# Optimization experiments

Measured on AMD Instinct MI355X. Metric: run time of the kernel, lower is better.

Reference implementation:

```python
import jax, jax.numpy as jnp
import numpy as np
from jax import lax

H = 512          # hidden_dim
U = H // 2       # GRU units per direction
L = 3            # num_layers
B = 64           # num sequences
T = 512          # timesteps per sequence
EXTRA = 1000     # pass-through tail rows in `states`
RATE = 0.1       # dropout_rate
WSCALE = 0.05


def setup_inputs() -> dict:
    key = jax.random.key(0)
    ks = jax.random.split(key, 9)
    N = B * T + EXTRA
    states = jax.random.normal(ks[0], (N, H), jnp.float32)
    # prefix-valid mask: each sequence has a random valid length in [1, T]
    lengths = jax.random.randint(ks[1], (B,), 1, T + 1)
    mask2d = jnp.arange(T)[None, :] < lengths[:, None]          # [B, T]
    mask = jnp.concatenate([mask2d.reshape(-1), jnp.zeros((EXTRA,), bool)])
    # per-layer, per-direction GRU params (Keras reset_after=True layout):
    # kernel [H, 3U] (z|r|h), recurrent [U, 3U], bias [2, 3U] (input bias, recurrent bias)
    Wf = jax.random.normal(ks[2], (L, H, 3 * U), jnp.float32) * WSCALE
    Uf = jax.random.normal(ks[3], (L, U, 3 * U), jnp.float32) * WSCALE
    bf = jnp.zeros((L, 2, 3 * U), jnp.float32)
    Wb = jax.random.normal(ks[4], (L, H, 3 * U), jnp.float32) * WSCALE
    Ub = jax.random.normal(ks[5], (L, U, 3 * U), jnp.float32) * WSCALE
    bb = jnp.zeros((L, 2, 3 * U), jnp.float32)
    return {
        "states": states, "mask": mask, "seq_shape": (B, T), "training": 1,
        "Wf": Wf, "Uf": Uf, "bf": bf, "Wb": Wb, "Ub": Ub, "bb": bb,
    }


def _gru_scan(x, m, W, Uw, b):
    """Keras GRU (reset_after=True) over time with Keras mask semantics.
    x: [T, B, H], m: [T, B] bool. Returns outputs [T, B, U].
    Masked steps carry state (output = previous output)."""
    bi, br = b[0], b[1]
    xp = jnp.einsum('tbh,hk->tbk', x, W) + bi   # [T, B, 3U], hoisted input proj
    h0 = jnp.zeros((x.shape[1], U), x.dtype)

    def step(h, inp):
        xp_t, m_t = inp
        hp = h @ Uw + br                         # [B, 3U]
        xz, xr, xh = jnp.split(xp_t, 3, axis=-1)
        hz, hr, hh = jnp.split(hp, 3, axis=-1)
        z = jax.nn.sigmoid(xz + hz)
        r = jax.nn.sigmoid(xr + hr)
        hcand = jnp.tanh(xh + r * hh)
        hn = z * h + (1.0 - z) * hcand
        hn = jnp.where(m_t[:, None], hn, h)      # carry state through masked steps
        return hn, hn

    _, ys = lax.scan(step, h0, (xp, m))
    return ys


def _forward(states, mask, seq_shape, training, Wf, Uf, bf, Wb, Ub, bb):
    Bn, Tn = int(seq_shape[0]), int(seq_shape[1])
    total = Bn * Tn
    x = states[:total].reshape(Bn, Tn, H).transpose(1, 0, 2)  # [T, B, H]
    m = mask[:total].reshape(Bn, Tn).T                        # [T, B]
    rate = RATE * float(bool(training))
    dkey = jax.random.key(1234)
    for l in range(L):
        yf = _gru_scan(x, m, Wf[l], Uf[l], bf[l])
        yb = jnp.flip(_gru_scan(jnp.flip(x, 0), jnp.flip(m, 0), Wb[l], Ub[l], bb[l]), 0)
        x = jnp.concatenate([yf, yb], axis=-1)                # [T, B, H]
        if rate > 0.0:
            dkey, sk = jax.random.split(dkey)
            keep = jax.random.bernoulli(sk, 1.0 - rate, x.shape)
            x = jnp.where(keep, x / (1.0 - rate), 0.0)
    out = x.transpose(1, 0, 2).reshape(-1, H)                 # [B*T, H]
    return jnp.concatenate([out, states[total:]], axis=0)


def reference(states, mask, seq_shape, training, Wf, Uf, bf, Wb, Ub, bb):
    return _forward(states, mask, seq_shape, training, Wf, Uf, bf, Wb, Ub, bb)
```

## Files before the change

kernel.cpp:

```cpp
#include <hip/hip_runtime.h>
#include <stdint.h>

typedef __attribute__((ext_vector_type(8))) short short8;
typedef __attribute__((ext_vector_type(4))) float f32x4;

#define XB16_OFF  0UL
#define XP_OFF    33554432UL
#define WT_OFF    134217728UL
#define UT_OFF    138936320UL
#define BIASC_OFF 141295616UL
#define BRC_OFF   141314048UL
#define MASKT_OFF 141332480UL
#define FLAG_OFF  141725760UL

#define HB_STRIDE 264
#define HBLK (16 * HB_STRIDE)
#define LDS_BYTES (((size_t)256 * HB_STRIDE + 2 * HBLK) * 2)

#define LDS_BARRIER() asm volatile("s_waitcnt lgkmcnt(0)\n\ts_barrier" ::: "memory")

__host__ __device__ static inline void tf2x32(unsigned k0, unsigned k1,
                                              unsigned x0, unsigned x1,
                                              unsigned* o0, unsigned* o1) {
  unsigned ks2 = k0 ^ k1 ^ 0x1BD11BDAu;
#define TFR(r) { x0 += x1; x1 = (x1 << (r)) | (x1 >> (32 - (r))); x1 ^= x0; }
  x0 += k0; x1 += k1;
  TFR(13) TFR(15) TFR(26) TFR(6)   x0 += k1;  x1 += ks2 + 1u;
  TFR(17) TFR(29) TFR(16) TFR(24)  x0 += ks2; x1 += k0 + 2u;
  TFR(13) TFR(15) TFR(26) TFR(6)   x0 += k0;  x1 += k1 + 3u;
  TFR(17) TFR(29) TFR(16) TFR(24)  x0 += k1;  x1 += ks2 + 4u;
  TFR(13) TFR(15) TFR(26) TFR(6)   x0 += ks2; x1 += k0 + 5u;
#undef TFR
  *o0 = x0; *o1 = x1;
}

__device__ static inline short f2bf(float f) {
  unsigned u = __float_as_uint(f);
  u = (u + 0x7fffu + ((u >> 16) & 1u)) >> 16;
  return (short)u;
}
__device__ static inline float bf2f(short s) {
  unsigned u = ((unsigned)(unsigned short)s) << 16;
  return __uint_as_float(u);
}
__device__ static inline float cvt_lo(unsigned d) {
  union { unsigned short u; _Float16 h; } c; c.u = (unsigned short)(d & 0xffffu);
  return (float)c.h;
}
__device__ static inline float cvt_hi(unsigned d) {
  union { unsigned short u; _Float16 h; } c; c.u = (unsigned short)(d >> 16);
  return (float)c.h;
}

__global__ void init_k(unsigned* flag) {
  if (threadIdx.x == 0) *flag = 0u;
}

__global__ __launch_bounds__(256) void prep_k(
    const float* __restrict__ states, const unsigned* __restrict__ maskw,
    const float* __restrict__ Wf, const float* __restrict__ Uf,
    const float* __restrict__ bf_, const float* __restrict__ Wb,
    const float* __restrict__ Ub, const float* __restrict__ bb_,
    short* __restrict__ xb16, float* __restrict__ dout,
    short* __restrict__ Wt, short* __restrict__ Ut,
    float* __restrict__ biasc, float* __restrict__ brc,
    unsigned* __restrict__ flag) {
  const unsigned gid = blockIdx.x * 256 + threadIdx.x;
  {
    unsigned c = gid & 511u, rw = gid >> 9;
    unsigned t = rw >> 6, b = rw & 63u;
    xb16[gid] = f2bf(states[(size_t)(b * 512 + t) * 512 + c]);
  }
  if (gid < 512000u) dout[16777216u + gid] = states[16777216u + gid];
  if (gid < 2359296u) {
    unsigned l = gid / 786432u, rem = gid % 786432u;
    unsigned n = rem >> 9, k = rem & 511u;
    float s = (n < 768u) ? Wf[(size_t)(l * 512 + k) * 768 + n]
                         : Wb[(size_t)(l * 512 + k) * 768 + (n - 768u)];
    Wt[gid] = f2bf(s);
  }
  if (gid < 1179648u) {
    unsigned g = gid / 196608u, rem = gid % 196608u;
    unsigned dirv = g / 3u, l = g % 3u;
    unsigned n = rem >> 8, k = rem & 255u;
    const float* Usrc = dirv ? Ub : Uf;
    Ut[gid] = f2bf(Usrc[(size_t)(l * 256 + k) * 768 + n]);
  }
  if (gid < 4608u) {
    unsigned l = gid / 1536u, n = gid % 1536u;
    unsigned dirv = n / 768u, rem = n % 768u;
    const float* bsrc = dirv ? bb_ : bf_;
    float v = bsrc[(l * 2 + 0) * 768 + rem];
    if (rem < 512u) v += bsrc[(l * 2 + 1) * 768 + rem];
    biasc[gid] = v;
  }
  if (gid < 4608u) {
    unsigned g = gid / 768u, n = gid % 768u;
    unsigned dirv = g / 3u, l = g % 3u;
    brc[gid] = (dirv ? bb_ : bf_)[(l * 2 + 1) * 768 + n];
  }
  if (gid < 8192u) {
    if (maskw[gid] > 1u) atomicOr(flag, 1u);
  }
}

__global__ __launch_bounds__(256) void maskt_k(
    const unsigned char* __restrict__ mask8, const unsigned* __restrict__ flagp,
    unsigned char* __restrict__ maskt) {
  const unsigned gid = blockIdx.x * 256 + threadIdx.x;
  const unsigned b = gid >> 9, t = gid & 511u;
  const bool mbyte = (*flagp) != 0u;
  unsigned v = mbyte ? (unsigned)mask8[gid] : ((const unsigned*)mask8)[gid];
  maskt[t * 64 + b] = v ? 1u : 0u;
}

__global__ __launch_bounds__(256) void proj_gemm(
    const short* __restrict__ A, const short* __restrict__ Bt,
    const float* __restrict__ bias, _Float16* __restrict__ C) {
  __shared__ __align__(16) short As[4096];
  __shared__ __align__(16) short Bs[4096];
  const int tid = threadIdx.x;
  const int wave = tid >> 6, lane = tid & 63;
  const int col = lane & 15, kq = lane >> 4;
  const int wr = wave >> 1, wc = wave & 1;
  const int m0 = blockIdx.x * 128, n0 = blockIdx.y * 128;
  const uint4* Aq = (const uint4*)A;
  const uint4* Bq = (const uint4*)Bt;
  uint4* AsQ = (uint4*)As;
  uint4* BsQ = (uint4*)Bs;
  f32x4 acc[4][4];
#pragma unroll
  for (int i = 0; i < 4; ++i)
#pragma unroll
    for (int j = 0; j < 4; ++j) acc[i][j] = (f32x4){0.f, 0.f, 0.f, 0.f};

  for (int kt = 0; kt < 16; ++kt) {
    const int k8 = kt * 4;
#pragma unroll
    for (int rnd = 0; rnd < 2; ++rnd) {
      int chunk = rnd * 256 + tid;
      int row = chunk >> 2, kc = chunk & 3;
      AsQ[chunk] = Aq[(size_t)(m0 + row) * 64 + k8 + kc];
      BsQ[chunk] = Bq[(size_t)(n0 + row) * 64 + k8 + kc];
    }
    __syncthreads();
    short8 af[4], bfv[4];
#pragma unroll
    for (int i = 0; i < 4; ++i)
      af[i] = *(const short8*)(As + (wr * 64 + i * 16 + col) * 32 + kq * 8);
#pragma unroll
    for (int j = 0; j < 4; ++j)
      bfv[j] = *(const short8*)(Bs + (wc * 64 + j * 16 + col) * 32 + kq * 8);
#pragma unroll
    for (int i = 0; i < 4; ++i)
#pragma unroll
      for (int j = 0; j < 4; ++j)
        acc[i][j] = __builtin_amdgcn_mfma_f32_16x16x32_bf16(af[i], bfv[j], acc[i][j], 0, 0, 0);
    __syncthreads();
  }
#pragma unroll
  for (int j = 0; j < 4; ++j) {
    const int cg = n0 + wc * 64 + j * 16 + col;
    const float bv = bias[cg];
    const int dirv = cg / 768, rem = cg % 768;
    const int gate = rem >> 8, u = rem & 255;
    const int w = u >> 4, c = u & 15;
    const int colofs = dirv * 768 +
        ((gate < 2) ? (w * 32 + c * 2 + gate) : (512 + w * 16 + c));
#pragma unroll
    for (int i = 0; i < 4; ++i) {
      const int rb = m0 + wr * 64 + i * 16 + kq * 4;
#pragma unroll
      for (int r = 0; r < 4; ++r)
        C[(size_t)(rb + r) * 1536 + colofs] = (_Float16)(acc[i][j][r] + bv);
    }
  }
}

__global__ __launch_bounds__(1024, 4) void gru16(
    const _Float16* __restrict__ xp, const short* __restrict__ UtAll,
    const float* __restrict__ brcAll, const unsigned char* __restrict__ maskt,
    short* __restrict__ yout, int layer) {
  extern __shared__ short lds[];
  short* hgate = lds;
  short* hbuf  = lds + 256 * HB_STRIDE;

  const int bid = blockIdx.x;
  const int dir = bid >> 2;
  const int b0 = (bid & 3) * 16;
  const int tid = threadIdx.x;
  const int wave = tid >> 6, lane = tid & 63;
  const int col = lane & 15, quad = lane >> 4;
  const int u = wave * 16 + col;
  const short* Ut = UtAll + (size_t)(dir * 3 + layer) * 768 * 256;
  const float* brc = brcAll + (dir * 3 + layer) * 768;

  const short* Uth = Ut + 512 * 256;
  for (int c = tid; c < 8192; c += 1024) {
    int row = c >> 5, q = c & 31;
    *(uint4*)(hgate + row * HB_STRIDE + q * 8) = *(const uint4*)(Uth + row * 256 + q * 8);
  }
  for (int i = tid; i < 2 * HBLK; i += 1024) hbuf[i] = 0;

  short8 zB[8], rB[8];
#pragma unroll
  for (int ks = 0; ks < 8; ++ks) {
    zB[ks] = *(const short8*)(Ut + (size_t)u * 256 + ks * 32 + quad * 8);
    rB[ks] = *(const short8*)(Ut + (size_t)(256 + u) * 256 + ks * 32 + quad * 8);
  }
  const float brh = brc[512 + u];

  const int t0 = dir ? 511 : 0;
  const int tstep = dir ? -1 : 1;
  const int xstep = tstep * 64 * 3072;
  const char* xpb = (const char*)xp;
  const int row0 = (t0 * 64 + b0 + quad * 4);
  unsigned xzrA = (unsigned)(row0 * 3072 + dir * 1536 + wave * 64 + col * 4);
  unsigned xzrB = xzrA + 6144u;
  unsigned xhA  = (unsigned)(row0 * 3072 + dir * 1536 + 1024 + wave * 32 + col * 2);
  unsigned xhB  = xhA + 6144u;

  const short* hgB = hgate + u * HB_STRIDE + quad * 8;
  const int rd_lane = col * HB_STRIDE + quad * 8;
  const int wr_lane = (quad * 4) * HB_STRIDE + u;

  unsigned yoff = (unsigned)(row0 * 1024 + dir * 512 + u * 2);
  const int ystep = tstep * 65536;
  int moff = t0 * 64 + b0 + quad * 4;

  unsigned pzr[4], ph[4], pmc;
  pzr[0] = *(const unsigned*)(xpb + xzrA);
  pzr[1] = *(const unsigned*)(xpb + xzrA + 3072);
  pzr[2] = *(const unsigned*)(xpb + xzrB);
  pzr[3] = *(const unsigned*)(xpb + xzrB + 3072);
  ph[0] = *(const unsigned short*)(xpb + xhA);
  ph[1] = *(const unsigned short*)(xpb + xhA + 3072);
  ph[2] = *(const unsigned short*)(xpb + xhB);
  ph[3] = *(const unsigned short*)(xpb + xhB + 3072);
  pmc = *(const unsigned*)(maskt + moff);

  float hp[4] = {0.f, 0.f, 0.f, 0.f};
  __syncthreads();

  for (int s = 0; s < 512; ++s) {
    f32x4 az, ar, ah;
#pragma unroll
    for (int r = 0; r < 4; ++r) {
      az[r] = cvt_lo(pzr[r]);
      ar[r] = cvt_hi(pzr[r]);
      ah[r] = brh;
    }
    if (s < 511) {
      xzrA += xstep; xzrB += xstep; xhA += xstep; xhB += xstep;
      pzr[0] = *(const unsigned*)(xpb + xzrA);
      pzr[1] = *(const unsigned*)(xpb + xzrA + 3072);
      pzr[2] = *(const unsigned*)(xpb + xzrB);
      pzr[3] = *(const unsigned*)(xpb + xzrB + 3072);
    }

    const short* hrd = hbuf + (s & 1) * HBLK + rd_lane;
#pragma unroll
    for (int ks = 0; ks < 8; ++ks) {
      short8 a  = *(const short8*)(hrd + ks * 32);
      short8 hb = *(const short8*)(hgB + ks * 32);
      az = __builtin_amdgcn_mfma_f32_16x16x32_bf16(a, zB[ks], az, 0, 0, 0);
      ar = __builtin_amdgcn_mfma_f32_16x16x32_bf16(a, rB[ks], ar, 0, 0, 0);
      ah = __builtin_amdgcn_mfma_f32_16x16x32_bf16(a, hb,     ah, 0, 0, 0);
    }

    short* hwr = hbuf + ((s & 1) ^ 1) * HBLK + wr_lane;
    char* yb = (char*)yout + yoff;
#pragma unroll
    for (int r = 0; r < 4; ++r) {
      float z  = 1.f / (1.f + __expf(-az[r]));
      float rr = 1.f / (1.f + __expf(-ar[r]));
      float xh = cvt_lo(ph[r]);
      float pre = xh + rr * ah[r];
      float hc = 1.f - 2.f / (__expf(2.f * pre) + 1.f);
      float hpv = hp[r];
      float hn = hc + z * (hpv - hc);
      hn = ((pmc >> (8 * r)) & 0xffu) ? hn : hpv;
      hp[r] = hn;
      short hnb = f2bf(hn);
      hwr[r * HB_STRIDE] = hnb;
      *(short*)(yb + r * 1024) = hnb;
    }
    yoff += ystep;
    if (s < 511) {
      ph[0] = *(const unsigned short*)(xpb + xhA);
      ph[1] = *(const unsigned short*)(xpb + xhA + 3072);
      ph[2] = *(const unsigned short*)(xpb + xhB);
      ph[3] = *(const unsigned short*)(xpb + xhB + 3072);
      moff += tstep * 64;
      pmc = *(const unsigned*)(maskt + moff);
    }
    LDS_BARRIER();
  }
}

__global__ __launch_bounds__(256) void drop_k(
    short* __restrict__ xb16, float* __restrict__ dout,
    const int* __restrict__ training, unsigned k0, unsigned k1, int last) {
  const unsigned gid = blockIdx.x * 256 + threadIdx.x;
  float v = bf2f(xb16[gid]);
  unsigned y0, y1;
  tf2x32(k0, k1, 0u, gid, &y0, &y1);
  unsigned bits = y0 ^ y1;
  float u = __uint_as_float((bits >> 9) | 0x3f800000u) - 1.0f;
  bool keep = u < 0.9f;
  int tr = *training;
  float ov = tr ? (keep ? v * (1.0f / 0.9f) : 0.0f) : v;
  if (last) {
    unsigned r = gid >> 9, c = gid & 511u;
    unsigned t = r >> 6, b = r & 63u;
    dout[(size_t)(b * 512 + t) * 512 + c] = ov;
  } else {
    xb16[gid] = f2bf(ov);
  }
}

extern "C" void kernel_launch(void* const* d_in, const int* in_sizes, int n_in,
                              void* d_out, int out_size, void* d_ws, size_t ws_size,
                              hipStream_t stream) {
  (void)in_sizes; (void)n_in; (void)out_size; (void)ws_size;
  const float* states = (const float*)d_in[0];
  const void*  mask   = d_in[1];
  const int*   training = (const int*)d_in[3];
  const float* Wf = (const float*)d_in[4];
  const float* Uf = (const float*)d_in[5];
  const float* bf_ = (const float*)d_in[6];
  const float* Wb = (const float*)d_in[7];
  const float* Ub = (const float*)d_in[8];
  const float* bb_ = (const float*)d_in[9];
  char* ws = (char*)d_ws;

  short* xb16   = (short*)(ws + XB16_OFF);
  _Float16* xp  = (_Float16*)(ws + XP_OFF);
  short* Wt     = (short*)(ws + WT_OFF);
  short* Ut     = (short*)(ws + UT_OFF);
  float* biasc  = (float*)(ws + BIASC_OFF);
  float* brc    = (float*)(ws + BRC_OFF);
  unsigned char* maskt = (unsigned char*)(ws + MASKT_OFF);
  unsigned* flag = (unsigned*)(ws + FLAG_OFF);
  float* dout = (float*)d_out;

  hipFuncSetAttribute((const void*)gru16,
                      hipFuncAttributeMaxDynamicSharedMemorySize, (int)LDS_BYTES);

  unsigned d0 = 0u, d1 = 1234u, sk0[3], sk1[3];
  for (int l = 0; l < 3; ++l) {
    unsigned a, b, c, d;
    tf2x32(d0, d1, 0u, 0u, &a, &b);
    tf2x32(d0, d1, 0u, 1u, &c, &d);
    sk0[l] = c; sk1[l] = d;
    d0 = a; d1 = b;
  }

  init_k<<<1, 64, 0, stream>>>(flag);
  prep_k<<<65536, 256, 0, stream>>>(states, (const unsigned*)mask, Wf, Uf, bf_,
                                    Wb, Ub, bb_, xb16, dout, Wt, Ut, biasc, brc, flag);
  maskt_k<<<128, 256, 0, stream>>>((const unsigned char*)mask, flag, maskt);
  for (int l = 0; l < 3; ++l) {
    proj_gemm<<<dim3(256, 12), 256, 0, stream>>>(xb16, Wt + (size_t)l * 1536 * 512,
                                                 biasc + l * 1536, xp);
    gru16<<<8, 1024, LDS_BYTES, stream>>>(xp, Ut, brc, maskt, xb16, l);
    drop_k<<<65536, 256, 0, stream>>>(xb16, dout, training, sk0[l], sk1[l], l == 2);
  }
}
```

Before: 4.129 ms.

## Transpose GRU recurrent MFMA so each lane owns four consecutive units

The recurrent matmul operands are swapped so weights become the A operand and the hidden state the B operand. Each lane now holds four consecutive hidden units for one sequence. The input projection GEMM writes its output in a matching per-timestep, per-direction layout, so each lane loads gate inputs with three 8-byte loads. Hidden-state writes to LDS and to the output are packed into one 8-byte store per lane using v_cvt_pk_bf16_f32, and the sigmoid and tanh now call exp2 directly. This is meant to cut the number of narrow scattered global loads and stores on the serial critical path. It relies on the GEMM epilogue and the GRU kernel agreeing on the new xp layout.

```diff
diff --git a/kernel.cpp b/kernel.cpp
--- a/kernel.cpp
+++ b/kernel.cpp
@@ -164,15 +164,13 @@
     const float bv = bias[cg];
     const int dirv = cg / 768, rem = cg % 768;
     const int gate = rem >> 8, u = rem & 255;
-    const int w = u >> 4, c = u & 15;
-    const int colofs = dirv * 768 +
-        ((gate < 2) ? (w * 32 + c * 2 + gate) : (512 + w * 16 + c));
+    const size_t cbase =
+        ((size_t)(((m0 >> 6) + wr) * 2 + dirv)) * 49152 + gate * 256 + u;
 #pragma unroll
     for (int i = 0; i < 4; ++i) {
-      const int rb = m0 + wr * 64 + i * 16 + kq * 4;
 #pragma unroll
       for (int r = 0; r < 4; ++r)
-        C[(size_t)(rb + r) * 1536 + colofs] = (_Float16)(acc[i][j][r] + bv);
+        C[cbase + (size_t)(i * 16 + kq * 4 + r) * 768] = (_Float16)(acc[i][j][r] + bv);
     }
   }
 }
@@ -191,7 +189,7 @@
   const int tid = threadIdx.x;
   const int wave = tid >> 6, lane = tid & 63;
   const int col = lane & 15, quad = lane >> 4;
-  const int u = wave * 16 + col;
+  const int u0 = wave * 16 + quad * 4;
   const short* Ut = UtAll + (size_t)(dir * 3 + layer) * 768 * 256;
   const float* brc = brcAll + (dir * 3 + layer) * 768;
 
@@ -202,98 +200,89 @@
   }
   for (int i = tid; i < 2 * HBLK; i += 1024) hbuf[i] = 0;
 
-  short8 zB[8], rB[8];
+  short8 zA[8], rA[8];
 #pragma unroll
   for (int ks = 0; ks < 8; ++ks) {
-    zB[ks] = *(const short8*)(Ut + (size_t)u * 256 + ks * 32 + quad * 8);
-    rB[ks] = *(const short8*)(Ut + (size_t)(256 + u) * 256 + ks * 32 + quad * 8);
-  }
-  const float brh = brc[512 + u];
+    zA[ks] = *(const short8*)(Ut + (size_t)(wave * 16 + col) * 256 + ks * 32 + quad * 8);
+    rA[ks] = *(const short8*)(Ut + (size_t)(256 + wave * 16 + col) * 256 + ks * 32 + quad * 8);
+  }
+  f32x4 brh;
+#pragma unroll
+  for (int r = 0; r < 4; ++r) brh[r] = brc[512 + u0 + r];
 
   const int t0 = dir ? 511 : 0;
   const int tstep = dir ? -1 : 1;
-  const int xstep = tstep * 64 * 3072;
   const char* xpb = (const char*)xp;
-  const int row0 = (t0 * 64 + b0 + quad * 4);
-  unsigned xzrA = (unsigned)(row0 * 3072 + dir * 1536 + wave * 64 + col * 4);
-  unsigned xzrB = xzrA + 6144u;
-  unsigned xhA  = (unsigned)(row0 * 3072 + dir * 1536 + 1024 + wave * 32 + col * 2);
-  unsigned xhB  = xhA + 6144u;
-
-  const short* hgB = hgate + u * HB_STRIDE + quad * 8;
+  const int gb = b0 + col;
+  unsigned xaddr = (unsigned)(((t0 * 2 + dir) * 64 + gb) * 1536 + wave * 32 + quad * 8);
+  const int xstep = tstep * 196608;
+
+  const short* hgA = hgate + (wave * 16 + col) * HB_STRIDE + quad * 8;
   const int rd_lane = col * HB_STRIDE + quad * 8;
-  const int wr_lane = (quad * 4) * HB_STRIDE + u;
-
-  unsigned yoff = (unsigned)(row0 * 1024 + dir * 512 + u * 2);
+  const int wr_lane = col * HB_STRIDE + u0;
+
+  unsigned yoff = (unsigned)((t0 * 64 + gb) * 1024 + dir * 512 + u0 * 2);
   const int ystep = tstep * 65536;
-  int moff = t0 * 64 + b0 + quad * 4;
-
-  unsigned pzr[4], ph[4], pmc;
-  pzr[0] = *(const unsigned*)(xpb + xzrA);
-  pzr[1] = *(const unsigned*)(xpb + xzrA + 3072);
-  pzr[2] = *(const unsigned*)(xpb + xzrB);
-  pzr[3] = *(const unsigned*)(xpb + xzrB + 3072);
-  ph[0] = *(const unsigned short*)(xpb + xhA);
-  ph[1] = *(const unsigned short*)(xpb + xhA + 3072);
-  ph[2] = *(const unsigned short*)(xpb + xhB);
-  ph[3] = *(const unsigned short*)(xpb + xhB + 3072);
-  pmc = *(const unsigned*)(maskt + moff);
+  int moff = t0 * 64 + gb;
+
+  uint2 pz, pr, ph;
+  unsigned pm;
+  pz = *(const uint2*)(xpb + xaddr);
+  pr = *(const uint2*)(xpb + xaddr + 512);
+  ph = *(const uint2*)(xpb + xaddr + 1024);
+  pm = maskt[moff];
 
   float hp[4] = {0.f, 0.f, 0.f, 0.f};
   __syncthreads();
 
   for (int s = 0; s < 512; ++s) {
     f32x4 az, ar, ah;
+    az[0] = cvt_lo(pz.x); az[1] = cvt_hi(pz.x);
+    az[2] = cvt_lo(pz.y); az[3] = cvt_hi(pz.y);
+    ar[0] = cvt_lo(pr.x); ar[1] = cvt_hi(pr.x);
+    ar[2] = cvt_lo(pr.y); ar[3] = cvt_hi(pr.y);
+    ah = brh;
+    float xh[4];
+    xh[0] = cvt_lo(ph.x); xh[1] = cvt_hi(ph.x);
+    xh[2] = cvt_lo(ph.y); xh[3] = cvt_hi(ph.y);
+    const bool mv = (pm != 0u);
+    if (s < 511) {
+      xaddr += xstep;
+      pz = *(const uint2*)(xpb + xaddr);
+      pr = *(const uint2*)(xpb + xaddr + 512);
+      ph = *(const uint2*)(xpb + xaddr + 1024);
+      moff += tstep * 64;
+      pm = maskt[moff];
+    }
+
+    const short* hrd = hbuf + (s & 1) * HBLK + rd_lane;
+#pragma unroll
+    for (int ks = 0; ks < 8; ++ks) {
+      short8 hbv = *(const short8*)(hrd + ks * 32);
+      short8 hg  = *(const short8*)(hgA + ks * 32);
+      az = __builtin_amdgcn_mfma_f32_16x16x32_bf16(zA[ks], hbv, az, 0, 0, 0);
+      ar = __builtin_amdgcn_mfma_f32_16x16x32_bf16(rA[ks], hbv, ar, 0, 0, 0);
+      ah = __builtin_amdgcn_mfma_f32_16x16x32_bf16(hg,     hbv, ah, 0, 0, 0);
+    }
+
+    float hn[4];
 #pragma unroll
     for (int r = 0; r < 4; ++r) {
-      az[r] = cvt_lo(pzr[r]);
-      ar[r] = cvt_hi(pzr[r]);
-      ah[r] = brh;
-    }
-    if (s < 511) {
-      xzrA += xstep; xzrB += xstep; xhA += xstep; xhB += xstep;
-      pzr[0] = *(const unsigned*)(xpb + xzrA);
-      pzr[1] = *(const unsigned*)(xpb + xzrA + 3072);
-      pzr[2] = *(const unsigned*)(xpb + xzrB);
-      pzr[3] = *(const unsigned*)(xpb + xzrB + 3072);
-    }
-
-    const short* hrd = hbuf + (s & 1) * HBLK + rd_lane;
-#pragma unroll
-    for (int ks = 0; ks < 8; ++ks) {
-      short8 a  = *(const short8*)(hrd + ks * 32);
-      short8 hb = *(const short8*)(hgB + ks * 32);
-      az = __builtin_amdgcn_mfma_f32_16x16x32_bf16(a, zB[ks], az, 0, 0, 0);
-      ar = __builtin_amdgcn_mfma_f32_16x16x32_bf16(a, rB[ks], ar, 0, 0, 0);
-      ah = __builtin_amdgcn_mfma_f32_16x16x32_bf16(a, hb,     ah, 0, 0, 0);
-    }
-
-    short* hwr = hbuf + ((s & 1) ^ 1) * HBLK + wr_lane;
-    char* yb = (char*)yout + yoff;
-#pragma unroll
-    for (int r = 0; r < 4; ++r) {
-      float z  = 1.f / (1.f + __expf(-az[r]));
-      float rr = 1.f / (1.f + __expf(-ar[r]));
-      float xh = cvt_lo(ph[r]);
-      float pre = xh + rr * ah[r];
-      float hc = 1.f - 2.f / (__expf(2.f * pre) + 1.f);
+      float z  = 1.f / (1.f + __builtin_amdgcn_exp2f(az[r] * -1.44269504f));
+      float rr = 1.f / (1.f + __builtin_amdgcn_exp2f(ar[r] * -1.44269504f));
+      float pre = xh[r] + rr * ah[r];
+      float hc = 1.f - 2.f / (__builtin_amdgcn_exp2f(pre * 2.88539008f) + 1.f);
       float hpv = hp[r];
-      float hn = hc + z * (hpv - hc);
-      hn = ((pmc >> (8 * r)) & 0xffu) ? hn : hpv;
-      hp[r] = hn;
-      short hnb = f2bf(hn);
-      hwr[r * HB_STRIDE] = hnb;
-      *(short*)(yb + r * 1024) = hnb;
-    }
+      float v = hc + z * (hpv - hc);
+      hn[r] = mv ? v : hpv;
+      hp[r] = hn[r];
+    }
+    uint2 packed;
+    asm("v_cvt_pk_bf16_f32 %0, %1, %2" : "=v"(packed.x) : "v"(hn[0]), "v"(hn[1]));
+    asm("v_cvt_pk_bf16_f32 %0, %1, %2" : "=v"(packed.y) : "v"(hn[2]), "v"(hn[3]));
+    *(uint2*)(hbuf + ((s & 1) ^ 1) * HBLK + wr_lane) = packed;
+    *(uint2*)((char*)yout + yoff) = packed;
     yoff += ystep;
-    if (s < 511) {
-      ph[0] = *(const unsigned short*)(xpb + xhA);
-      ph[1] = *(const unsigned short*)(xpb + xhA + 3072);
-      ph[2] = *(const unsigned short*)(xpb + xhB);
-      ph[3] = *(const unsigned short*)(xpb + xhB + 3072);
-      moff += tstep * 64;
-      pmc = *(const unsigned*)(maskt + moff);
-    }
     LDS_BARRIER();
   }
 }
```

Result: faster. 3.797 ms (-8.0%).
